# Performance work log

Hardware: AMD Instinct MI355X
Metric: run time of the kernel (lower is better)

## Reference

```python
import jax, jax.numpy as jnp
import numpy as np

B, S, T, H, VS, VT = 64, 64, 64, 1024, 32000, 32000


def _init(key, shape, scale=0.05):
    return scale * jax.random.normal(key, shape, dtype=jnp.float32)


def setup_inputs() -> dict:
    key = jax.random.key(0)
    ks = jax.random.split(key, 16)
    source = jax.random.randint(ks[0], (B, S), 0, VS)
    target = jax.random.randint(ks[1], (B, T), 0, VT)
    emb_src = _init(ks[2], (VS, H)).at[0].set(0.0)   # padding_idx=0
    emb_tgt = _init(ks[3], (VT, H)).at[0].set(0.0)   # padding_idx=0
    W_ih_enc = _init(ks[4], (4 * H, H)); W_hh_enc = _init(ks[5], (4 * H, H))
    b_ih_enc = _init(ks[6], (4 * H,));   b_hh_enc = _init(ks[7], (4 * H,))
    W_ih_dec = _init(ks[8], (4 * H, H)); W_hh_dec = _init(ks[9], (4 * H, H))
    b_ih_dec = _init(ks[10], (4 * H,));  b_hh_dec = _init(ks[11], (4 * H,))
    W_att = _init(ks[12], (H, 2 * H));   b_att = _init(ks[13], (H,))
    W_out = _init(ks[14], (VT, H));      b_out = _init(ks[15], (VT,))
    return dict(source=source, target=target, emb_src=emb_src, emb_tgt=emb_tgt,
                W_ih_enc=W_ih_enc, W_hh_enc=W_hh_enc, b_ih_enc=b_ih_enc, b_hh_enc=b_hh_enc,
                W_ih_dec=W_ih_dec, W_hh_dec=W_hh_dec, b_ih_dec=b_ih_dec, b_hh_dec=b_hh_dec,
                W_att=W_att, b_att=b_att, W_out=W_out, b_out=b_out)


def _lstm_cell(x, h, c, W_ih, W_hh, b):
    # PyTorch gate order: i, f, g, o
    gates = x @ W_ih.T + h @ W_hh.T + b
    i, f, g, o = jnp.split(gates, 4, axis=-1)
    c_new = jax.nn.sigmoid(f) * c + jax.nn.sigmoid(i) * jnp.tanh(g)
    h_new = jax.nn.sigmoid(o) * jnp.tanh(c_new)
    return h_new, c_new


def reference(source, target, emb_src, emb_tgt,
              W_ih_enc, W_hh_enc, b_ih_enc, b_hh_enc,
              W_ih_dec, W_hh_dec, b_ih_dec, b_hh_dec,
              W_att, b_att, W_out, b_out):
    src = source.T              # [S, B]
    tgt = target.T              # [T, B]
    h0 = jnp.zeros((B, H), jnp.float32)
    c0 = jnp.zeros((B, H), jnp.float32)

    # ---- Encoder: time-major LSTM via scan (dropout in eval mode = identity) ----
    x_src = emb_src[src]        # [S, B, H]
    b_enc = b_ih_enc + b_hh_enc

    def enc_step(carry, x_t):
        h, c = carry
        h, c = _lstm_cell(x_t, h, c, W_ih_enc, W_hh_enc, b_enc)
        return (h, c), h

    (hT, cT), hx_list = jax.lax.scan(enc_step, (h0, c0), x_src)  # hx_list: [S, B, H]

    # ---- Decoder: hx_cx is never updated in the original loop, so every
    # timestep uses the SAME encoder final state -> fully vectorizable over t ----
    words_f = tgt[: S - 1]      # [Td, B], Td = T-1 (S == T)
    words_t = tgt[1:]           # [Td, B]
    x_dec = emb_tgt[words_f]    # [Td, B, H]
    b_dec = b_ih_dec + b_hh_dec
    gates = x_dec @ W_ih_dec.T + (hT @ W_hh_dec.T + b_dec)[None]  # [Td, B, 4H]
    i, f, g, o = jnp.split(gates, 4, axis=-1)
    c_new = jax.nn.sigmoid(f) * cT[None] + jax.nn.sigmoid(i) * jnp.tanh(g)
    hx = jax.nn.sigmoid(o) * jnp.tanh(c_new)                       # [Td, B, H]

    # ---- Attention (dot-product over source positions, softmax over S) ----
    scores = jnp.einsum('tbh,sbh->tsb', hx, hx_list)               # [Td, S, B]
    neg_inf = jnp.asarray(-jnp.inf, jnp.float32)
    mask = (src != 0)[None]                                        # [1, S, B]
    scores = jnp.where(mask, scores, neg_inf)
    align = jax.nn.softmax(scores, axis=1)                         # over S
    content = jnp.einsum('tsb,sbh->tbh', align, hx_list)           # [Td, B, H]
    concat = jnp.concatenate([content, hx], axis=-1)               # [Td, B, 2H]
    hx_att = jnp.tanh(concat @ W_att.T + b_att)                    # [Td, B, H]

    # ---- Output projection + per-step cross entropy (ignore_index=0), summed ----
    logits = hx_att @ W_out.T + b_out                              # [Td, B, VT]
    logp = jax.nn.log_softmax(logits, axis=-1)
    nll = -jnp.take_along_axis(logp, words_t[..., None], axis=-1).squeeze(-1)  # [Td, B]
    valid = (words_t != 0).astype(jnp.float32)
    per_step = jnp.sum(nll * valid, axis=1) / jnp.maximum(jnp.sum(valid, axis=1), 1.0)
    return jnp.sum(per_step)
```

## Files before the change

### kernel.cpp

```cpp
#include <hip/hip_runtime.h>
#include <math.h>

#define Bb 64
#define Ss 64
#define Hh 1024
#define Vv 32000
#define RD 4032
#define RP 4096
#define NT4 4096
#define ENC_NBLK 64

typedef unsigned short u16;
typedef unsigned long long u64;
typedef __attribute__((ext_vector_type(8))) short bf16x8;
typedef __attribute__((ext_vector_type(4))) float f32x4;

#define MFMA(a, b, c) __builtin_amdgcn_mfma_f32_16x16x32_bf16(a, b, c, 0, 0, 0)

__device__ __forceinline__ u16 f2b(float f) {
  union { float f; unsigned u; } v; v.f = f;
  unsigned r = v.u + 0x7fffu + ((v.u >> 16) & 1u);
  return (u16)(r >> 16);
}
__device__ __forceinline__ float b2f(u16 b) {
  union { unsigned u; float f; } v; v.u = ((unsigned)b) << 16; return v.f;
}
__device__ __forceinline__ float sigf(float x) { return 1.f / (1.f + expf(-x)); }

__device__ __forceinline__ void gll16(const void* g, void* l) {
  __builtin_amdgcn_global_load_lds(
      (const __attribute__((address_space(1))) unsigned int*)g,
      (__attribute__((address_space(3))) unsigned int*)l, 16, 0, 0);
}

__global__ void k_fail(float* out) { out[0] = 1e30f; }

__global__ void k_cvt(const float* __restrict__ in, u16* __restrict__ out, int n4) {
  int i = blockIdx.x * blockDim.x + threadIdx.x;
  const int st = gridDim.x * blockDim.x;
  for (; i < n4; i += st) {
    float4 v = ((const float4*)in)[i];
    ushort4 o; o.x = f2b(v.x); o.y = f2b(v.y); o.z = f2b(v.z); o.w = f2b(v.w);
    ((ushort4*)out)[i] = o;
  }
}

__global__ void k_gather(const int* __restrict__ tok, const float* __restrict__ emb,
                         u16* __restrict__ outp, int nstep) {
  const int r = blockIdx.x;
  const int step = r >> 6, b = r & 63;
  const int idx = (step < nstep) ? tok[b * 64 + step] : 0;
  const float4 v = ((const float4*)(emb + (size_t)idx * Hh))[threadIdx.x];
  ushort4 o; o.x = f2b(v.x); o.y = f2b(v.y); o.z = f2b(v.z); o.w = f2b(v.w);
  ((ushort4*)(outp + (size_t)r * Hh))[threadIdx.x] = o;
}

template<int EPI>
__global__ __launch_bounds__(256)
void k_gemm(const u16* __restrict__ A, const u16* __restrict__ Bm,
            float* __restrict__ C, int M, int N, int K,
            const float* __restrict__ bias, int act,
            float* __restrict__ pmax, float* __restrict__ psum, int ncols) {
  __shared__ __align__(16) u16 As[128 * 64];
  __shared__ __align__(16) u16 Bs[128 * 64];
  const int tid = threadIdx.x;
  const int wave = tid >> 6, lane = tid & 63;
  const int l15 = lane & 15, lhi = lane >> 4;
  int bx = blockIdx.x, by = blockIdx.y;
  {
    const int gx_ = gridDim.x, gy_ = gridDim.y;
    const int nwg = gx_ * gy_;
    if ((gy_ & 3) == 0 && (gx_ & 1) == 0) {
      const int f = by * gx_ + bx;
      const int x = f & 7, i = f >> 3;
      const int rby = gy_ >> 2, hx = gx_ >> 1;
      by = (x >> 1) * rby + (i % rby);
      bx = (x & 1) * hx + (i / rby);
    } else if ((nwg & 7) == 0) {
      int flat = by * gx_ + bx;
      const int qq = nwg >> 3;
      flat = (flat & 7) * qq + (flat >> 3);
      bx = flat % gx_; by = flat / gx_;
    }
  }
  const int m0 = by * 128, n0 = bx * 128;
  const int wm = (wave >> 1) * 64, wn = (wave & 1) * 64;
  f32x4 acc[4][4] = {};

  const int srow = wave * 32 + (lane >> 3);
  const int scolb = (lane & 7) * 16;

  for (int k0 = 0; k0 < K; k0 += 64) {
    __syncthreads();
#pragma unroll
    for (int q = 0; q < 4; ++q) {
      const int r = srow + q * 8;
      int ra = m0 + r; ra = (ra < M) ? ra : (M - 1);
      const char* ga = (const char*)(A + (size_t)ra * K + k0) + scolb;
      const char* gb = (const char*)(Bm + (size_t)(n0 + r) * K + k0) + scolb;
      char* lA = (char*)As + (wave * 32 + q * 8) * 128;
      char* lB = (char*)Bs + (wave * 32 + q * 8) * 128;
      gll16(ga, lA);
      gll16(gb, lB);
    }
    __syncthreads();
#pragma unroll
    for (int kk = 0; kk < 2; ++kk) {
      const int ko = kk * 32 + lhi * 8;
      bf16x8 af[4], bfr[4];
#pragma unroll
      for (int i = 0; i < 4; ++i) af[i] = *(const bf16x8*)(As + (wm + i * 16 + l15) * 64 + ko);
#pragma unroll
      for (int j = 0; j < 4; ++j) bfr[j] = *(const bf16x8*)(Bs + (wn + j * 16 + l15) * 64 + ko);
#pragma unroll
      for (int i = 0; i < 4; ++i)
#pragma unroll
        for (int j = 0; j < 4; ++j)
          acc[i][j] = MFMA(af[i], bfr[j], acc[i][j]);
    }
  }

  if (EPI == 0) {
#pragma unroll
    for (int i = 0; i < 4; ++i) {
      const int gr = m0 + wm + i * 16 + lhi * 4;
#pragma unroll
      for (int j = 0; j < 4; ++j) {
        const int gc = n0 + wn + j * 16 + l15;
        const float bv = bias ? bias[gc] : 0.f;
#pragma unroll
        for (int rr = 0; rr < 4; ++rr) {
          float v = acc[i][j][rr] + bv;
          if (act) v = tanhf(v);
          C[(size_t)(gr + rr) * N + gc] = v;
        }
      }
    }
  } else {
    float bj[4];
#pragma unroll
    for (int j = 0; j < 4; ++j) bj[j] = bias[n0 + wn + j * 16 + l15];
    const int pc = bx * 2 + (wn ? 1 : 0);
#pragma unroll
    for (int i = 0; i < 4; ++i) {
#pragma unroll
      for (int rr = 0; rr < 4; ++rr) {
        float v0 = acc[i][0][rr] + bj[0];
        float v1 = acc[i][1][rr] + bj[1];
        float v2 = acc[i][2][rr] + bj[2];
        float v3 = acc[i][3][rr] + bj[3];
        float m = fmaxf(fmaxf(v0, v1), fmaxf(v2, v3));
#pragma unroll
        for (int d = 1; d < 16; d <<= 1) m = fmaxf(m, __shfl_xor(m, d, 64));
        float s = __expf(v0 - m) + __expf(v1 - m) + __expf(v2 - m) + __expf(v3 - m);
#pragma unroll
        for (int d = 1; d < 16; d <<= 1) s += __shfl_xor(s, d, 64);
        if (l15 == 0) {
          const int grow = m0 + wm + i * 16 + lhi * 4 + rr;
          pmax[(size_t)grow * ncols + pc] = m;
          psum[(size_t)grow * ncols + pc] = s;
        }
      }
    }
  }
}

__global__ __launch_bounds__(256, 1)
void k_enc_all(const u16* __restrict__ Wb, const float* __restrict__ gx,
               const float* __restrict__ b_ih, const float* __restrict__ b_hh,
               u16* __restrict__ hxl, float* __restrict__ c_out, int* flags) {
  __shared__ __align__(16) u16 Ws[64 * 1024];
  __shared__ float Gs[64 * 65];
  __shared__ float bsum[64];
  const int tid = threadIdx.x;
  const int wave = tid >> 6, lane = tid & 63;
  const int l15 = lane & 15, lhi = lane >> 4;
  const int c0 = blockIdx.x * 16;
  const int cb = tid >> 2, cq = tid & 3;
  const int rot = blockIdx.x & 31;

  for (int i = tid; i < 64 * 128; i += 256) {
    const int r = i >> 7, ck = i & 127;
    const int grow = (r >> 4) * Hh + c0 + (r & 15);
    const int bo = (ck * 16) ^ ((r & 7) << 4);
    *(bf16x8*)((char*)Ws + r * 2048 + bo) = *(const bf16x8*)(Wb + (size_t)grow * Hh + ck * 8);
  }
  if (tid < 64) {
    const int col = (tid >> 4) * Hh + c0 + (tid & 15);
    bsum[tid] = b_ih[col] + b_hh[col];
  }
  float creg[4] = {0.f, 0.f, 0.f, 0.f};
  __syncthreads();

  for (int s = 0; s < 64; ++s) {
    float4 ga[4];
#pragma unroll
    for (int g = 0; g < 4; ++g)
      ga[g] = *(const float4*)(gx + (size_t)(s * 64 + cb) * NT4 + g * Hh + c0 + cq * 4);

    f32x4 acc[4] = {};
    if (s > 0) {
      if (wave == 0) {
        for (;;) {
          const int f = __hip_atomic_load(flags + lane * 4,
                                          __ATOMIC_RELAXED, __HIP_MEMORY_SCOPE_AGENT);
          if (__all(f >= s)) break;
          __builtin_amdgcn_s_sleep(1);
        }
      }
      __syncthreads();
      const u64* apw = (const u64*)(hxl + ((size_t)(s - 1) * 64 + wave * 16 + l15) * Hh);
      const char* wsb = (const char*)Ws;
      const int xr = (l15 & 7) << 4;
#pragma unroll 8
      for (int i = 0; i < 32; ++i) {
        const int kf = (i + rot) & 31;
        const int k = kf * 32 + lhi * 8;
        const u64 ua = __hip_atomic_load(apw + (k >> 2), __ATOMIC_RELAXED,
                                         __HIP_MEMORY_SCOPE_AGENT);
        const u64 ub = __hip_atomic_load(apw + (k >> 2) + 1, __ATOMIC_RELAXED,
                                         __HIP_MEMORY_SCOPE_AGENT);
        union { u64 qq[2]; bf16x8 v; } cv;
        cv.qq[0] = ua; cv.qq[1] = ub;
        const int kb = (k * 2) ^ xr;
#pragma unroll
        for (int nt = 0; nt < 4; ++nt) {
          const bf16x8 bfrag = *(const bf16x8*)(wsb + (nt * 16 + l15) * 2048 + kb);
          acc[nt] = MFMA(cv.v, bfrag, acc[nt]);
        }
      }
    }
#pragma unroll
    for (int nt = 0; nt < 4; ++nt)
#pragma unroll
      for (int r = 0; r < 4; ++r)
        Gs[(wave * 16 + lhi * 4 + r) * 65 + nt * 16 + l15] = acc[nt][r];
    __syncthreads();
    {
      const float* gsrow = Gs + cb * 65;
      u64 pk = 0;
#pragma unroll
      for (int j = 0; j < 4; ++j) {
        const int col = cq * 4 + j;
        const float gi = gsrow[col]      + ga[0][j] + bsum[col];
        const float gf = gsrow[16 + col] + ga[1][j] + bsum[16 + col];
        const float gg = gsrow[32 + col] + ga[2][j] + bsum[32 + col];
        const float go = gsrow[48 + col] + ga[3][j] + bsum[48 + col];
        const float cn = sigf(gf) * creg[j] + sigf(gi) * tanhf(gg);
        const float hv = sigf(go) * tanhf(cn);
        creg[j] = cn;
        pk |= (u64)f2b(hv) << (16 * j);
      }
      __hip_atomic_store((u64*)(hxl + ((size_t)s * 64 + cb) * Hh + c0 + cq * 4), pk,
                         __ATOMIC_RELAXED, __HIP_MEMORY_SCOPE_AGENT);
    }
    __syncthreads();
    if (tid == 0)
      __hip_atomic_store(flags + blockIdx.x * 4, s + 1,
                         __ATOMIC_RELAXED, __HIP_MEMORY_SCOPE_AGENT);
  }
#pragma unroll
  for (int j = 0; j < 4; ++j)
    c_out[cb * Hh + c0 + cq * 4 + j] = creg[j];
}

__global__ void k_dec_cell(const float* __restrict__ G, const float* __restrict__ dbase,
                           const float* __restrict__ cT, const float* __restrict__ b_ih,
                           const float* __restrict__ b_hh, u16* __restrict__ Acat) {
  const int idx = blockIdx.x * 256 + threadIdx.x;
  if (idx >= RD * Hh) return;
  const int r = idx >> 10, nh = idx & 1023;
  const int b = r & 63;
  const size_t gr = (size_t)r * NT4;
  const size_t br = (size_t)b * NT4;
  const float gi = G[gr + nh]        + dbase[br + nh]        + b_ih[nh]        + b_hh[nh];
  const float gf = G[gr + Hh + nh]   + dbase[br + Hh + nh]   + b_ih[Hh + nh]   + b_hh[Hh + nh];
  const float gg = G[gr + 2*Hh + nh] + dbase[br + 2*Hh + nh] + b_ih[2*Hh + nh] + b_hh[2*Hh + nh];
  const float go = G[gr + 3*Hh + nh] + dbase[br + 3*Hh + nh] + b_ih[3*Hh + nh] + b_hh[3*Hh + nh];
  const float cn = sigf(gf) * cT[b * Hh + nh] + sigf(gi) * tanhf(gg);
  const float hv = sigf(go) * tanhf(cn);
  Acat[(size_t)r * 2048 + Hh + nh] = f2b(hv);
}

__global__ __launch_bounds__(256)
void k_attn(u16* Acat, const u16* __restrict__ hxl, const int* __restrict__ src) {
  __shared__ float qs[Hh];
  __shared__ float sc[Ss];
  const int r = blockIdx.x;
  const int b = r & 63;
  const int tid = threadIdx.x, wave = tid >> 6, lane = tid & 63;
  for (int h = tid; h < Hh; h += 256) qs[h] = b2f(Acat[(size_t)r * 2048 + Hh + h]);
  __syncthreads();
  for (int sub = 0; sub < 16; ++sub) {
    const int ss = wave * 16 + sub;
    const ushort4* hp4 = (const ushort4*)(hxl + ((size_t)ss * Bb + b) * Hh);
    float p = 0.f;
#pragma unroll
    for (int q = 0; q < 4; ++q) {
      const int i4 = lane + 64 * q;
      const ushort4 v = hp4[i4];
      p += qs[i4 * 4 + 0] * b2f(v.x) + qs[i4 * 4 + 1] * b2f(v.y)
         + qs[i4 * 4 + 2] * b2f(v.z) + qs[i4 * 4 + 3] * b2f(v.w);
    }
#pragma unroll
    for (int d = 1; d < 64; d <<= 1) p += __shfl_xor(p, d, 64);
    if (lane == 0) sc[ss] = (src[b * 64 + ss] != 0) ? p : -INFINITY;
  }
  __syncthreads();
  if (wave == 0) {
    const float v = sc[lane];
    float m = v;
#pragma unroll
    for (int d = 1; d < 64; d <<= 1) m = fmaxf(m, __shfl_xor(m, d, 64));
    const float e = __expf(v - m);
    float ssum = e;
#pragma unroll
    for (int d = 1; d < 64; d <<= 1) ssum += __shfl_xor(ssum, d, 64);
    sc[lane] = e / ssum;
  }
  __syncthreads();
  float4 a4 = {0.f, 0.f, 0.f, 0.f};
  for (int s2 = 0; s2 < 64; ++s2) {
    const float a = sc[s2];
    const ushort4 v = *(const ushort4*)(hxl + ((size_t)s2 * Bb + b) * Hh + tid * 4);
    a4.x += a * b2f(v.x); a4.y += a * b2f(v.y);
    a4.z += a * b2f(v.z); a4.w += a * b2f(v.w);
  }
  u16* dst = Acat + (size_t)r * 2048 + tid * 4;
  dst[0] = f2b(a4.x); dst[1] = f2b(a4.y); dst[2] = f2b(a4.z); dst[3] = f2b(a4.w);
}

__global__ void k_lse(const float* __restrict__ pmax, const float* __restrict__ psum,
                      float* __restrict__ lse, int ncols) {
  const int r = blockIdx.x * 4 + (threadIdx.x >> 6);
  const int lane = threadIdx.x & 63;
  if (r >= RD) return;
  float m = -INFINITY;
  for (int i = lane; i < ncols; i += 64) m = fmaxf(m, pmax[(size_t)r * ncols + i]);
#pragma unroll
  for (int d = 1; d < 64; d <<= 1) m = fmaxf(m, __shfl_xor(m, d, 64));
  float s = 0.f;
  for (int i = lane; i < ncols; i += 64)
    s += psum[(size_t)r * ncols + i] * __expf(pmax[(size_t)r * ncols + i] - m);
#pragma unroll
  for (int d = 1; d < 64; d <<= 1) s += __shfl_xor(s, d, 64);
  if (lane == 0) lse[r] = m + logf(s);
}

__global__ void k_tlogit(const float* __restrict__ hx_att, const int* __restrict__ target,
                         const float* __restrict__ W, const float* __restrict__ bo,
                         float* __restrict__ outp) {
  const int r = blockIdx.x * 4 + (threadIdx.x >> 6);
  const int lane = threadIdx.x & 63;
  if (r >= RD) return;
  const int t = r >> 6, b = r & 63;
  const int w = target[b * 64 + t + 1];
  const float* a = hx_att + (size_t)r * Hh;
  const float* wr = W + (size_t)w * Hh;
  float p = 0.f;
  for (int h = lane; h < Hh; h += 64) p += a[h] * wr[h];
#pragma unroll
  for (int d = 1; d < 64; d <<= 1) p += __shfl_xor(p, d, 64);
  if (lane == 0) outp[r] = p + bo[w];
}

__global__ void k_final(const float* __restrict__ lse, const float* __restrict__ tl,
                        const int* __restrict__ target, float* __restrict__ out) {
  const int t = threadIdx.x;
  float ps = 0.f;
  if (t < 63) {
    float sn = 0.f, cnt = 0.f;
    for (int b = 0; b < 64; ++b) {
      const int r = t * 64 + b;
      const int w = target[b * 64 + t + 1];
      if (w != 0) { sn += lse[r] - tl[r]; cnt += 1.f; }
    }
    ps = sn / fmaxf(cnt, 1.f);
  }
#pragma unroll
  for (int d = 1; d < 64; d <<= 1) ps += __shfl_xor(ps, d, 64);
  if (t == 0) out[0] = ps;
}

extern "C" void kernel_launch(void* const* d_in, const int* in_sizes, int n_in,
                              void* d_out, int out_size, void* d_ws, size_t ws_size,
                              hipStream_t stream) {
  const int*   source   = (const int*)d_in[0];
  const int*   target   = (const int*)d_in[1];
  const float* emb_src  = (const float*)d_in[2];
  const float* emb_tgt  = (const float*)d_in[3];
  const float* W_ih_enc = (const float*)d_in[4];
  const float* W_hh_enc = (const float*)d_in[5];
  const float* b_ih_enc = (const float*)d_in[6];
  const float* b_hh_enc = (const float*)d_in[7];
  const float* W_ih_dec = (const float*)d_in[8];
  const float* W_hh_dec = (const float*)d_in[9];
  const float* b_ih_dec = (const float*)d_in[10];
  const float* b_hh_dec = (const float*)d_in[11];
  const float* W_att    = (const float*)d_in[12];
  const float* b_att    = (const float*)d_in[13];
  const float* W_out    = (const float*)d_in[14];
  const float* b_out    = (const float*)d_in[15];
  float* out = (float*)d_out;

  char* base = (char*)d_ws;
  size_t off = 0;
  auto alloc = [&](size_t bytes) -> void* {
    void* r = base + off; off += (bytes + 255) & ~(size_t)255; return r;
  };
  u16*   wb_ih_enc = (u16*)alloc((size_t)NT4 * Hh * 2);
  u16*   wb_hh_enc = (u16*)alloc((size_t)NT4 * Hh * 2);
  u16*   wb_ih_dec = (u16*)alloc((size_t)NT4 * Hh * 2);
  u16*   wb_hh_dec = (u16*)alloc((size_t)NT4 * Hh * 2);
  u16*   wb_att    = (u16*)alloc((size_t)Hh * 2048 * 2);
  u16*   wb_out    = (u16*)alloc((size_t)Vv * Hh * 2);
  u16*   x_src_b   = (u16*)alloc((size_t)RP * Hh * 2);
  u16*   x_dec_b   = (u16*)alloc((size_t)RP * Hh * 2);
  float* gates     = (float*)alloc((size_t)RP * NT4 * 4);
  u16*   hxl       = (u16*)alloc((size_t)Ss * Bb * Hh * 2);
  float* c_enc     = (float*)alloc((size_t)Bb * Hh * 4);
  float* dbase     = (float*)alloc((size_t)128 * NT4 * 4);
  u16*   Acat      = (u16*)alloc((size_t)RP * 2048 * 2);
  float* hx_att    = (float*)alloc((size_t)RP * Hh * 4);
  u16*   hx_att_b  = (u16*)alloc((size_t)RP * Hh * 2);
  float* pmax      = (float*)alloc((size_t)RP * 500 * 4);
  float* psum      = (float*)alloc((size_t)RP * 500 * 4);
  float* lse       = (float*)alloc((size_t)RD * 4);
  float* tlog      = (float*)alloc((size_t)RD * 4);
  int*   flags     = (int*)alloc(ENC_NBLK * 16);

  if (off > ws_size) { k_fail<<<1, 1, 0, stream>>>(out); return; }

  k_cvt<<<2048, 256, 0, stream>>>(W_ih_enc, wb_ih_enc, NT4 * Hh / 4);
  k_cvt<<<2048, 256, 0, stream>>>(W_hh_enc, wb_hh_enc, NT4 * Hh / 4);
  k_cvt<<<2048, 256, 0, stream>>>(W_ih_dec, wb_ih_dec, NT4 * Hh / 4);
  k_cvt<<<2048, 256, 0, stream>>>(W_hh_dec, wb_hh_dec, NT4 * Hh / 4);
  k_cvt<<<2048, 256, 0, stream>>>(W_att, wb_att, Hh * 2048 / 4);
  k_cvt<<<2048, 256, 0, stream>>>(W_out, wb_out, Vv * Hh / 4);

  hipMemsetAsync(flags, 0, ENC_NBLK * 16, stream);

  k_gather<<<RP, 256, 0, stream>>>(source, emb_src, x_src_b, 64);
  k_gather<<<RP, 256, 0, stream>>>(target, emb_tgt, x_dec_b, 63);

  k_gemm<0><<<dim3(32, 32), 256, 0, stream>>>(x_src_b, wb_ih_enc, gates, RP, NT4, Hh,
                                              nullptr, 0, nullptr, nullptr, 0);
  k_enc_all<<<ENC_NBLK, 256, 0, stream>>>(wb_hh_enc, gates, b_ih_enc, b_hh_enc,
                                          hxl, c_enc, flags);

  k_gemm<0><<<dim3(32, 32), 256, 0, stream>>>(x_dec_b, wb_ih_dec, gates, RP, NT4, Hh,
                                              nullptr, 0, nullptr, nullptr, 0);
  k_gemm<0><<<dim3(32, 1), 256, 0, stream>>>(hxl + (size_t)63 * Bb * Hh, wb_hh_dec, dbase,
                                             64, NT4, Hh, nullptr, 0, nullptr, nullptr, 0);
  k_dec_cell<<<(RD * Hh) / 256, 256, 0, stream>>>(gates, dbase, c_enc, b_ih_dec, b_hh_dec, Acat);

  k_attn<<<RD, 256, 0, stream>>>(Acat, hxl, source);

  k_gemm<0><<<dim3(8, 32), 256, 0, stream>>>(Acat, wb_att, hx_att, RP, Hh, 2048,
                                             b_att, 1, nullptr, nullptr, 0);
  k_cvt<<<2048, 256, 0, stream>>>(hx_att, hx_att_b, RP * Hh / 4);

  k_gemm<2><<<dim3(250, 32), 256, 0, stream>>>(hx_att_b, wb_out, nullptr, RP, Vv, Hh,
                                               b_out, 0, pmax, psum, 500);
  k_lse<<<(RD + 3) / 4, 256, 0, stream>>>(pmax, psum, lse, 500);
  k_tlogit<<<(RD + 3) / 4, 256, 0, stream>>>(hx_att, target, W_out, b_out, tlog);
  k_final<<<1, 64, 0, stream>>>(lse, tlog, target, out);
}
```

Baseline: 1.546 ms.

## Overlap decoder input GEMM with encoder recurrence and use bf16 intermediates

The encoder recurrence kernel gains extra blocks that compute the decoder input-gate GEMM concurrently, so the idle GPU compute during the serial 64-step scan is used. Per-block flag synchronisation is replaced by sentinel-filled hidden-state buffers: each wave polls its own h values until no sentinel remains, and prefetches the next step's h into registers. Gate pre-activations and the attention output are stored as bf16 instead of fp32, the tanh is fused into the attention GEMM epilogue (which removes a conversion kernel), and the decoder cell is vectorised. The sentinel scheme depends on a real bf16 pair never equalling all-ones and adds a large memset. Storing the gates in bf16 adds rounding error.

```diff
diff --git a/kernel.cpp b/kernel.cpp
--- a/kernel.cpp
+++ b/kernel.cpp
@@ -9,6 +9,7 @@
 #define RP 4096
 #define NT4 4096
 #define ENC_NBLK 64
+#define SENT 0xFFFFFFFFFFFFFFFFULL
 
 typedef unsigned short u16;
 typedef unsigned long long u64;
@@ -26,6 +27,13 @@
   union { unsigned u; float f; } v; v.u = ((unsigned)b) << 16; return v.f;
 }
 __device__ __forceinline__ float sigf(float x) { return 1.f / (1.f + expf(-x)); }
+
+__device__ __forceinline__ u64 AL(const u64* p) {
+  return __hip_atomic_load(p, __ATOMIC_RELAXED, __HIP_MEMORY_SCOPE_AGENT);
+}
+__device__ __forceinline__ void AS(u64* p, u64 v) {
+  __hip_atomic_store(p, v, __ATOMIC_RELAXED, __HIP_MEMORY_SCOPE_AGENT);
+}
 
 __device__ __forceinline__ void gll16(const void* g, void* l) {
   __builtin_amdgcn_global_load_lds(
@@ -55,11 +63,69 @@
   ((ushort4*)(outp + (size_t)r * Hh))[threadIdx.x] = o;
 }
 
+__device__ __forceinline__ void dg_tile(const u16* __restrict__ A, const u16* __restrict__ Bm,
+                                        u16* __restrict__ C, int bx, int by,
+                                        u16* As, u16* Bs) {
+  const int tid = threadIdx.x;
+  const int wave = tid >> 6, lane = tid & 63;
+  const int l15 = lane & 15, lhi = lane >> 4;
+  const int m0 = by * 128, n0 = bx * 128;
+  const int wm = (wave >> 1) * 64, wn = (wave & 1) * 64;
+  f32x4 acc[4][4] = {};
+  const int srow = wave * 32 + (lane >> 3);
+  const int scolb = (lane & 7) * 16;
+  for (int k0 = 0; k0 < Hh; k0 += 64) {
+    __syncthreads();
+#pragma unroll
+    for (int q = 0; q < 4; ++q) {
+      const int r = srow + q * 8;
+      gll16((const char*)(A + (size_t)(m0 + r) * Hh + k0) + scolb,
+            (char*)As + (wave * 32 + q * 8) * 128);
+      gll16((const char*)(Bm + (size_t)(n0 + r) * Hh + k0) + scolb,
+            (char*)Bs + (wave * 32 + q * 8) * 128);
+    }
+    __syncthreads();
+#pragma unroll
+    for (int kk = 0; kk < 2; ++kk) {
+      const int ko = kk * 32 + lhi * 8;
+      bf16x8 af[4], bfr[4];
+#pragma unroll
+      for (int i = 0; i < 4; ++i) af[i] = *(const bf16x8*)(As + (wm + i * 16 + l15) * 64 + ko);
+#pragma unroll
+      for (int j = 0; j < 4; ++j) bfr[j] = *(const bf16x8*)(Bs + (wn + j * 16 + l15) * 64 + ko);
+#pragma unroll
+      for (int i = 0; i < 4; ++i)
+#pragma unroll
+        for (int j = 0; j < 4; ++j)
+          acc[i][j] = MFMA(af[i], bfr[j], acc[i][j]);
+    }
+  }
+#pragma unroll
+  for (int i = 0; i < 4; ++i) {
+    const int gr = m0 + wm + i * 16 + lhi * 4;
+#pragma unroll
+    for (int j = 0; j < 4; ++j) {
+      const int gc = n0 + wn + j * 16 + l15;
+#pragma unroll
+      for (int rr = 0; rr < 4; ++rr)
+        C[(size_t)(gr + rr) * NT4 + gc] = f2b(acc[i][j][rr]);
+    }
+  }
+}
+
+__global__ __launch_bounds__(256)
+void k_pre(const u16* __restrict__ A, const u16* __restrict__ Bm, u16* __restrict__ C) {
+  __shared__ __align__(16) u16 As[128 * 64];
+  __shared__ __align__(16) u16 Bs[128 * 64];
+  const int t = blockIdx.x;
+  dg_tile(A, Bm, C, t & 31, t >> 5, As, Bs);
+}
+
 template<int EPI>
 __global__ __launch_bounds__(256)
 void k_gemm(const u16* __restrict__ A, const u16* __restrict__ Bm,
-            float* __restrict__ C, int M, int N, int K,
-            const float* __restrict__ bias, int act,
+            void* __restrict__ C, int M, int N, int K,
+            const float* __restrict__ bias,
             float* __restrict__ pmax, float* __restrict__ psum, int ncols) {
   __shared__ __align__(16) u16 As[128 * 64];
   __shared__ __align__(16) u16 Bs[128 * 64];
@@ -86,7 +152,6 @@
   const int m0 = by * 128, n0 = bx * 128;
   const int wm = (wave >> 1) * 64, wn = (wave & 1) * 64;
   f32x4 acc[4][4] = {};
-
   const int srow = wave * 32 + (lane >> 3);
   const int scolb = (lane & 7) * 16;
 
@@ -96,12 +161,10 @@
     for (int q = 0; q < 4; ++q) {
       const int r = srow + q * 8;
       int ra = m0 + r; ra = (ra < M) ? ra : (M - 1);
-      const char* ga = (const char*)(A + (size_t)ra * K + k0) + scolb;
-      const char* gb = (const char*)(Bm + (size_t)(n0 + r) * K + k0) + scolb;
-      char* lA = (char*)As + (wave * 32 + q * 8) * 128;
-      char* lB = (char*)Bs + (wave * 32 + q * 8) * 128;
-      gll16(ga, lA);
-      gll16(gb, lB);
+      gll16((const char*)(A + (size_t)ra * K + k0) + scolb,
+            (char*)As + (wave * 32 + q * 8) * 128);
+      gll16((const char*)(Bm + (size_t)(n0 + r) * K + k0) + scolb,
+            (char*)Bs + (wave * 32 + q * 8) * 128);
     }
     __syncthreads();
 #pragma unroll
@@ -129,11 +192,21 @@
         const int gc = n0 + wn + j * 16 + l15;
         const float bv = bias ? bias[gc] : 0.f;
 #pragma unroll
-        for (int rr = 0; rr < 4; ++rr) {
-          float v = acc[i][j][rr] + bv;
-          if (act) v = tanhf(v);
-          C[(size_t)(gr + rr) * N + gc] = v;
-        }
+        for (int rr = 0; rr < 4; ++rr)
+          ((float*)C)[(size_t)(gr + rr) * N + gc] = acc[i][j][rr] + bv;
+      }
+    }
+  } else if (EPI == 3) {
+#pragma unroll
+    for (int i = 0; i < 4; ++i) {
+      const int gr = m0 + wm + i * 16 + lhi * 4;
+#pragma unroll
+      for (int j = 0; j < 4; ++j) {
+        const int gc = n0 + wn + j * 16 + l15;
+        const float bv = bias[gc];
+#pragma unroll
+        for (int rr = 0; rr < 4; ++rr)
+          ((u16*)C)[(size_t)(gr + rr) * N + gc] = f2b(tanhf(acc[i][j][rr] + bv));
       }
     }
   } else {
@@ -166,13 +239,23 @@
 }
 
 __global__ __launch_bounds__(256, 1)
-void k_enc_all(const u16* __restrict__ Wb, const float* __restrict__ gx,
-               const float* __restrict__ b_ih, const float* __restrict__ b_hh,
-               u16* __restrict__ hxl, float* __restrict__ c_out, int* flags) {
-  __shared__ __align__(16) u16 Ws[64 * 1024];
-  __shared__ float Gs[64 * 65];
-  __shared__ float bsum[64];
+void k_enc_fused(const u16* __restrict__ Wb, const u16* __restrict__ gx,
+                 const float* __restrict__ b_ih, const float* __restrict__ b_hh,
+                 u16* __restrict__ hxl, float* __restrict__ c_out,
+                 const u16* __restrict__ Adec, const u16* __restrict__ Bdec,
+                 u16* __restrict__ Cdec) {
+  __shared__ __align__(16) char LB[64 * 2048 + 64 * 65 * 4 + 256];
   const int tid = threadIdx.x;
+
+  if (blockIdx.x >= ENC_NBLK) {
+    const int t = blockIdx.x - ENC_NBLK;
+    dg_tile(Adec, Bdec, Cdec, t & 31, t >> 5, (u16*)LB, (u16*)(LB + 16384));
+    return;
+  }
+
+  u16* Ws = (u16*)LB;
+  float* Gs = (float*)(LB + 131072);
+  float* bsum = (float*)(LB + 131072 + 64 * 65 * 4);
   const int wave = tid >> 6, lane = tid & 63;
   const int l15 = lane & 15, lhi = lane >> 4;
   const int c0 = blockIdx.x * 16;
@@ -192,42 +275,38 @@
   float creg[4] = {0.f, 0.f, 0.f, 0.f};
   __syncthreads();
 
+  u64 ha[32], hb[32];
   for (int s = 0; s < 64; ++s) {
-    float4 ga[4];
+    u64 graw[4];
 #pragma unroll
     for (int g = 0; g < 4; ++g)
-      ga[g] = *(const float4*)(gx + (size_t)(s * 64 + cb) * NT4 + g * Hh + c0 + cq * 4);
+      graw[g] = *(const u64*)(gx + (size_t)(s * 64 + cb) * NT4 + g * Hh + c0 + cq * 4);
 
     f32x4 acc[4] = {};
     if (s > 0) {
-      if (wave == 0) {
-        for (;;) {
-          const int f = __hip_atomic_load(flags + lane * 4,
-                                          __ATOMIC_RELAXED, __HIP_MEMORY_SCOPE_AGENT);
-          if (__all(f >= s)) break;
-          __builtin_amdgcn_s_sleep(1);
+      const u64* apw = (const u64*)(hxl + ((size_t)(s - 1) * 64 + wave * 16 + l15) * Hh);
+      for (;;) {
+        bool any = false;
+#pragma unroll
+        for (int i = 0; i < 32; ++i) {
+          const int kw = ((i + rot) & 31) * 8 + lhi * 2;
+          if (ha[i] == SENT) { ha[i] = AL(apw + kw); any = true; }
+          if (hb[i] == SENT) { hb[i] = AL(apw + kw + 1); any = true; }
         }
-      }
-      __syncthreads();
-      const u64* apw = (const u64*)(hxl + ((size_t)(s - 1) * 64 + wave * 16 + l15) * Hh);
+        if (!__any(any)) break;
+        __builtin_amdgcn_s_sleep(1);
+      }
       const char* wsb = (const char*)Ws;
       const int xr = (l15 & 7) << 4;
-#pragma unroll 8
+#pragma unroll
       for (int i = 0; i < 32; ++i) {
         const int kf = (i + rot) & 31;
-        const int k = kf * 32 + lhi * 8;
-        const u64 ua = __hip_atomic_load(apw + (k >> 2), __ATOMIC_RELAXED,
-                                         __HIP_MEMORY_SCOPE_AGENT);
-        const u64 ub = __hip_atomic_load(apw + (k >> 2) + 1, __ATOMIC_RELAXED,
-                                         __HIP_MEMORY_SCOPE_AGENT);
-        union { u64 qq[2]; bf16x8 v; } cv;
-        cv.qq[0] = ua; cv.qq[1] = ub;
-        const int kb = (k * 2) ^ xr;
-#pragma unroll
-        for (int nt = 0; nt < 4; ++nt) {
-          const bf16x8 bfrag = *(const bf16x8*)(wsb + (nt * 16 + l15) * 2048 + kb);
-          acc[nt] = MFMA(cv.v, bfrag, acc[nt]);
-        }
+        union { u64 q[2]; bf16x8 v; } cv;
+        cv.q[0] = ha[i]; cv.q[1] = hb[i];
+        const int kb = ((kf * 32 + lhi * 8) * 2) ^ xr;
+#pragma unroll
+        for (int nt = 0; nt < 4; ++nt)
+          acc[nt] = MFMA(cv.v, *(const bf16x8*)(wsb + (nt * 16 + l15) * 2048 + kb), acc[nt]);
       }
     }
 #pragma unroll
@@ -242,44 +321,61 @@
 #pragma unroll
       for (int j = 0; j < 4; ++j) {
         const int col = cq * 4 + j;
-        const float gi = gsrow[col]      + ga[0][j] + bsum[col];
-        const float gf = gsrow[16 + col] + ga[1][j] + bsum[16 + col];
-        const float gg = gsrow[32 + col] + ga[2][j] + bsum[32 + col];
-        const float go = gsrow[48 + col] + ga[3][j] + bsum[48 + col];
+        const float gi = gsrow[col]      + b2f((u16)(graw[0] >> (16 * j))) + bsum[col];
+        const float gf = gsrow[16 + col] + b2f((u16)(graw[1] >> (16 * j))) + bsum[16 + col];
+        const float gg = gsrow[32 + col] + b2f((u16)(graw[2] >> (16 * j))) + bsum[32 + col];
+        const float go = gsrow[48 + col] + b2f((u16)(graw[3] >> (16 * j))) + bsum[48 + col];
         const float cn = sigf(gf) * creg[j] + sigf(gi) * tanhf(gg);
         const float hv = sigf(go) * tanhf(cn);
         creg[j] = cn;
         pk |= (u64)f2b(hv) << (16 * j);
       }
-      __hip_atomic_store((u64*)(hxl + ((size_t)s * 64 + cb) * Hh + c0 + cq * 4), pk,
-                         __ATOMIC_RELAXED, __HIP_MEMORY_SCOPE_AGENT);
+      AS((u64*)(hxl + ((size_t)s * 64 + cb) * Hh + c0 + cq * 4), pk);
+    }
+    if (s < 63) {
+      const u64* apn = (const u64*)(hxl + ((size_t)s * 64 + wave * 16 + l15) * Hh);
+#pragma unroll
+      for (int i = 0; i < 32; ++i) {
+        const int kw = ((i + rot) & 31) * 8 + lhi * 2;
+        ha[i] = AL(apn + kw);
+        hb[i] = AL(apn + kw + 1);
+      }
     }
     __syncthreads();
-    if (tid == 0)
-      __hip_atomic_store(flags + blockIdx.x * 4, s + 1,
-                         __ATOMIC_RELAXED, __HIP_MEMORY_SCOPE_AGENT);
   }
 #pragma unroll
   for (int j = 0; j < 4; ++j)
     c_out[cb * Hh + c0 + cq * 4 + j] = creg[j];
 }
 
-__global__ void k_dec_cell(const float* __restrict__ G, const float* __restrict__ dbase,
+__global__ void k_dec_cell(const u16* __restrict__ G, const float* __restrict__ dbase,
                            const float* __restrict__ cT, const float* __restrict__ b_ih,
                            const float* __restrict__ b_hh, u16* __restrict__ Acat) {
   const int idx = blockIdx.x * 256 + threadIdx.x;
-  if (idx >= RD * Hh) return;
-  const int r = idx >> 10, nh = idx & 1023;
+  const int r = idx >> 8, c4 = (idx & 255) * 4;
+  if (r >= RD) return;
   const int b = r & 63;
-  const size_t gr = (size_t)r * NT4;
-  const size_t br = (size_t)b * NT4;
-  const float gi = G[gr + nh]        + dbase[br + nh]        + b_ih[nh]        + b_hh[nh];
-  const float gf = G[gr + Hh + nh]   + dbase[br + Hh + nh]   + b_ih[Hh + nh]   + b_hh[Hh + nh];
-  const float gg = G[gr + 2*Hh + nh] + dbase[br + 2*Hh + nh] + b_ih[2*Hh + nh] + b_hh[2*Hh + nh];
-  const float go = G[gr + 3*Hh + nh] + dbase[br + 3*Hh + nh] + b_ih[3*Hh + nh] + b_hh[3*Hh + nh];
-  const float cn = sigf(gf) * cT[b * Hh + nh] + sigf(gi) * tanhf(gg);
-  const float hv = sigf(go) * tanhf(cn);
-  Acat[(size_t)r * 2048 + Hh + nh] = f2b(hv);
+  u64 graw[4]; f32x4 dv[4], bi[4], bh[4];
+#pragma unroll
+  for (int g = 0; g < 4; ++g) {
+    graw[g] = *(const u64*)(G + (size_t)r * NT4 + g * Hh + c4);
+    dv[g] = *(const f32x4*)(dbase + (size_t)b * NT4 + g * Hh + c4);
+    bi[g] = *(const f32x4*)(b_ih + g * Hh + c4);
+    bh[g] = *(const f32x4*)(b_hh + g * Hh + c4);
+  }
+  const f32x4 cv4 = *(const f32x4*)(cT + b * Hh + c4);
+  u64 pk = 0;
+#pragma unroll
+  for (int j = 0; j < 4; ++j) {
+    const float gi = b2f((u16)(graw[0] >> (16 * j))) + dv[0][j] + bi[0][j] + bh[0][j];
+    const float gf = b2f((u16)(graw[1] >> (16 * j))) + dv[1][j] + bi[1][j] + bh[1][j];
+    const float gg = b2f((u16)(graw[2] >> (16 * j))) + dv[2][j] + bi[2][j] + bh[2][j];
+    const float go = b2f((u16)(graw[3] >> (16 * j))) + dv[3][j] + bi[3][j] + bh[3][j];
+    const float cn = sigf(gf) * cv4[j] + sigf(gi) * tanhf(gg);
+    const float hv = sigf(go) * tanhf(cn);
+    pk |= (u64)f2b(hv) << (16 * j);
+  }
+  *(u64*)(Acat + (size_t)r * 2048 + Hh + c4) = pk;
 }
 
 __global__ __launch_bounds__(256)
@@ -347,7 +443,7 @@
   if (lane == 0) lse[r] = m + logf(s);
 }
 
-__global__ void k_tlogit(const float* __restrict__ hx_att, const int* __restrict__ target,
+__global__ void k_tlogit(const u16* __restrict__ hx_att_b, const int* __restrict__ target,
                          const float* __restrict__ W, const float* __restrict__ bo,
                          float* __restrict__ outp) {
   const int r = blockIdx.x * 4 + (threadIdx.x >> 6);
@@ -355,10 +451,10 @@
   if (r >= RD) return;
   const int t = r >> 6, b = r & 63;
   const int w = target[b * 64 + t + 1];
-  const float* a = hx_att + (size_t)r * Hh;
+  const u16* a = hx_att_b + (size_t)r * Hh;
   const float* wr = W + (size_t)w * Hh;
   float p = 0.f;
-  for (int h = lane; h < Hh; h += 64) p += a[h] * wr[h];
+  for (int h = lane; h < Hh; h += 64) p += b2f(a[h]) * wr[h];
 #pragma unroll
   for (int d = 1; d < 64; d <<= 1) p += __shfl_xor(p, d, 64);
   if (lane == 0) outp[r] = p + bo[w];
@@ -416,18 +512,17 @@
   u16*   wb_out    = (u16*)alloc((size_t)Vv * Hh * 2);
   u16*   x_src_b   = (u16*)alloc((size_t)RP * Hh * 2);
   u16*   x_dec_b   = (u16*)alloc((size_t)RP * Hh * 2);
-  float* gates     = (float*)alloc((size_t)RP * NT4 * 4);
+  u16*   gates16   = (u16*)alloc((size_t)RP * NT4 * 2);
+  u16*   gates_dec = (u16*)alloc((size_t)RP * NT4 * 2);
   u16*   hxl       = (u16*)alloc((size_t)Ss * Bb * Hh * 2);
   float* c_enc     = (float*)alloc((size_t)Bb * Hh * 4);
-  float* dbase     = (float*)alloc((size_t)128 * NT4 * 4);
+  float* dbase     = (float*)alloc((size_t)64 * NT4 * 4);
   u16*   Acat      = (u16*)alloc((size_t)RP * 2048 * 2);
-  float* hx_att    = (float*)alloc((size_t)RP * Hh * 4);
   u16*   hx_att_b  = (u16*)alloc((size_t)RP * Hh * 2);
   float* pmax      = (float*)alloc((size_t)RP * 500 * 4);
   float* psum      = (float*)alloc((size_t)RP * 500 * 4);
   float* lse       = (float*)alloc((size_t)RD * 4);
   float* tlog      = (float*)alloc((size_t)RD * 4);
-  int*   flags     = (int*)alloc(ENC_NBLK * 16);
 
   if (off > ws_size) { k_fail<<<1, 1, 0, stream>>>(out); return; }
 
@@ -438,31 +533,28 @@
   k_cvt<<<2048, 256, 0, stream>>>(W_att, wb_att, Hh * 2048 / 4);
   k_cvt<<<2048, 256, 0, stream>>>(W_out, wb_out, Vv * Hh / 4);
 
-  hipMemsetAsync(flags, 0, ENC_NBLK * 16, stream);
+  hipMemsetAsync(hxl, 0xFF, (size_t)Ss * Bb * Hh * 2, stream);
 
   k_gather<<<RP, 256, 0, stream>>>(source, emb_src, x_src_b, 64);
   k_gather<<<RP, 256, 0, stream>>>(target, emb_tgt, x_dec_b, 63);
 
-  k_gemm<0><<<dim3(32, 32), 256, 0, stream>>>(x_src_b, wb_ih_enc, gates, RP, NT4, Hh,
-                                              nullptr, 0, nullptr, nullptr, 0);
-  k_enc_all<<<ENC_NBLK, 256, 0, stream>>>(wb_hh_enc, gates, b_ih_enc, b_hh_enc,
-                                          hxl, c_enc, flags);
-
-  k_gemm<0><<<dim3(32, 32), 256, 0, stream>>>(x_dec_b, wb_ih_dec, gates, RP, NT4, Hh,
-                                              nullptr, 0, nullptr, nullptr, 0);
+  k_pre<<<1024, 256, 0, stream>>>(x_src_b, wb_ih_enc, gates16);
+
+  k_enc_fused<<<ENC_NBLK + 1024, 256, 0, stream>>>(wb_hh_enc, gates16, b_ih_enc, b_hh_enc,
+                                                   hxl, c_enc, x_dec_b, wb_ih_dec, gates_dec);
+
   k_gemm<0><<<dim3(32, 1), 256, 0, stream>>>(hxl + (size_t)63 * Bb * Hh, wb_hh_dec, dbase,
-                                             64, NT4, Hh, nullptr, 0, nullptr, nullptr, 0);
-  k_dec_cell<<<(RD * Hh) / 256, 256, 0, stream>>>(gates, dbase, c_enc, b_ih_dec, b_hh_dec, Acat);
+                                             64, NT4, Hh, nullptr, nullptr, nullptr, 0);
+  k_dec_cell<<<RD, 256, 0, stream>>>(gates_dec, dbase, c_enc, b_ih_dec, b_hh_dec, Acat);
 
   k_attn<<<RD, 256, 0, stream>>>(Acat, hxl, source);
 
-  k_gemm<0><<<dim3(8, 32), 256, 0, stream>>>(Acat, wb_att, hx_att, RP, Hh, 2048,
-                                             b_att, 1, nullptr, nullptr, 0);
-  k_cvt<<<2048, 256, 0, stream>>>(hx_att, hx_att_b, RP * Hh / 4);
+  k_gemm<3><<<dim3(8, 32), 256, 0, stream>>>(Acat, wb_att, hx_att_b, RP, Hh, 2048,
+                                             b_att, nullptr, nullptr, 0);
 
   k_gemm<2><<<dim3(250, 32), 256, 0, stream>>>(hx_att_b, wb_out, nullptr, RP, Vv, Hh,
-                                               b_out, 0, pmax, psum, 500);
+                                               b_out, pmax, psum, 500);
   k_lse<<<(RD + 3) / 4, 256, 0, stream>>>(pmax, psum, lse, 500);
-  k_tlogit<<<(RD + 3) / 4, 256, 0, stream>>>(hx_att, target, W_out, b_out, tlog);
+  k_tlogit<<<(RD + 3) / 4, 256, 0, stream>>>(hx_att_b, target, W_out, b_out, tlog);
   k_final<<<1, 64, 0, stream>>>(lse, tlog, target, out);
 }
```

Result: slower. 1.847 ms (+19.5%).
